# Optimization experiments

Measured on AMD Instinct MI355X. Metric: run time of the kernel, lower is better.

## Reference

```python
import jax, jax.numpy as jnp
import numpy as np

N, F, C, H, D = 32768, 128, 4, 8, 32
DM = H * D  # 256, d_model
E, B = 65536, 8192


def _pe():
    # sinusoidal positional encoding over the chain dimension, shape [C, DM]
    pos = jnp.arange(C, dtype=jnp.float32)[:, None]
    di = jnp.arange(0, DM, 2, dtype=jnp.float32)[None, :]
    div = 10000.0 ** (di / DM)
    pe = jnp.zeros((C, DM), jnp.float32)
    pe = pe.at[:, 0::2].set(jnp.sin(pos / div))
    pe = pe.at[:, 1::2].set(jnp.cos(pos / div))
    return pe


def _leaky(v):
    return jnp.where(v >= 0, v, 0.2 * v)


def setup_inputs() -> dict:
    key = jax.random.key(0)
    ks = jax.random.split(key, 6)
    x = jax.random.normal(ks[0], (N, F), jnp.float32)
    edge_index = jax.random.randint(ks[1], (2, E), 0, N)
    bridge_index = jax.random.randint(ks[2], (2, B), 0, N)
    W_in = jax.random.normal(ks[3], (DM, F), jnp.float32) * 0.05       # linear_input.weight
    double_attn = jax.random.normal(ks[4], (1, C * H, D), jnp.float32) * 0.1
    W_res = jax.random.normal(ks[5], (C * DM, F), jnp.float32) * 0.05  # residual_linear.weight
    bias = jnp.zeros((C * DM,), jnp.float32)
    prelu_w = jnp.float32(0.25)  # nn.PReLU default
    return {"x": x, "edge_index": edge_index, "bridge_index": bridge_index,
            "W_in": W_in, "double_attn": double_attn, "W_res": W_res,
            "bias": bias, "prelu_w": prelu_w}


def reference(x, edge_index, bridge_index, W_in, double_attn, W_res, bias, prelu_w):
    n = x.shape[0]
    # project + chain positional encoding -> [n, C, H, D]
    xl = x @ W_in.T                                   # [n, DM]
    xr = (xl[:, None, :] + _pe()[None]).reshape(n, C, H, D)

    src_bond, dst_bond = edge_index[0], edge_index[1]
    bond_attn = _leaky(xr[src_bond] + xr[dst_bond])   # [E, C, H, D]

    src_bridge, dst_bridge = bridge_index[0], bridge_index[1]
    ch = jnp.arange(C)
    prev_ch = jnp.clip(ch - 1, 0, None)
    next_ch = jnp.clip(ch + 1, None, C - 1)
    src2dst = _leaky(xr[dst_bridge] + xr[src_bridge][:, next_ch]).at[:, -1].set(0.0)
    dst2src = _leaky(xr[src_bridge] + xr[dst_bridge][:, prev_ch]).at[:, 0].set(0.0)

    full_src = jnp.concatenate([src_bond, src_bridge, dst_bridge])   # [Et]
    full_dst = jnp.concatenate([dst_bond, dst_bridge, src_bridge])   # [Et]
    x_src = jnp.concatenate([xr[src_bond], xr[src_bridge], xr[dst_bridge]], axis=0).reshape(-1, C * H, D)
    edge_attn = jnp.concatenate([bond_attn, src2dst, dst2src], axis=0).reshape(-1, C * H, D)

    scores = (double_attn * edge_attn).sum(-1)        # [Et, C*H]
    exp_s = jnp.exp(scores - scores.max())            # global-max stabilized, as in original
    denom = jax.ops.segment_sum(exp_s, full_dst, num_segments=n)     # [n, C*H]
    alpha = exp_s / (denom[full_dst] + 1e-16)

    # NOTE: faithful to original bug - x_src (per-edge, len Et) indexed by NODE ids
    proj = x_src[full_src] * alpha[..., None]         # [Et, C*H, D]
    out = jax.ops.segment_sum(proj, full_dst, num_segments=n)        # [n, C*H, D]

    out = out + (x @ W_res.T).reshape(n, C * H, D)    # residual
    out = out.reshape(n, C * H * D) + bias            # concat + bias
    out = jnp.where(out >= 0, out, prelu_w * out)     # PReLU
    return out
```

## Files before the change

kernel.cpp:

```cpp
#include <hip/hip_runtime.h>
#include <math.h>

#define N_NODES 32768
#define F_IN    128
#define C_CH    4
#define H_HEADS 8
#define D_DIM   32
#define DM      256
#define E_BOND  65536
#define B_BRIDGE 8192
#define ET      (E_BOND + 2*B_BRIDGE)
#define OUTC    1024
#define CAP     24
#define NCOLS   1280

#define WS_XL      0u
#define WS_PE      33554432u
#define WS_SCORES  33558528u
#define WS_BUCKET2 44044288u
#define WS_CNT     50335744u
#define WS_GMAX    50466816u
#define WS_RESID   50470912u
#define WS_XB      117579776u
#define WS_WC      125968384u

typedef __attribute__((ext_vector_type(8))) short bf16x8;
typedef __attribute__((ext_vector_type(4))) float f32x4;
typedef __attribute__((ext_vector_type(4))) _Float16 f16x4;

__device__ __forceinline__ unsigned enc_f32(float f) {
    unsigned u = __float_as_uint(f);
    return (u & 0x80000000u) ? ~u : (u | 0x80000000u);
}
__device__ __forceinline__ float dec_f32(unsigned u) {
    return (u & 0x80000000u) ? __uint_as_float(u & 0x7fffffffu) : __uint_as_float(~u);
}
__device__ __forceinline__ float leaky(float v) { return v >= 0.f ? v : 0.2f*v; }
__device__ __forceinline__ ushort f2bf(float f) {
    unsigned u = __float_as_uint(f);
    unsigned r = (u + 0x7fffu + ((u >> 16) & 1u)) >> 16;
    return (ushort)r;
}

__device__ __forceinline__ void edge_decode(int e, const int* __restrict__ ei,
                                            const int* __restrict__ bi,
                                            int& nA, int& nB, int& tp) {
    if (e < E_BOND)               { nA = ei[e]; nB = ei[E_BOND + e]; tp = 0; }
    else if (e < E_BOND+B_BRIDGE) { int i = e - E_BOND;
                                    nA = bi[B_BRIDGE + i]; nB = bi[i]; tp = 1; }
    else                          { int i = e - E_BOND - B_BRIDGE;
                                    nA = bi[i]; nB = bi[B_BRIDGE + i]; tp = 2; }
}

__global__ void pe_init_kernel(float* __restrict__ pe, unsigned* __restrict__ gmax) {
    int tid = threadIdx.x;
    int c = tid >> 8, p = tid & 255;
    float expo = (float)(p & ~1) * (1.0f/256.0f);
    float div  = powf(10000.0f, expo);
    float arg  = (float)c / div;
    pe[tid] = (p & 1) ? cosf(arg) : sinf(arg);
    if (tid == 0) *gmax = 0u;
}

__global__ __launch_bounds__(256) void cvt_x_kernel(const float* __restrict__ x,
                                                    ushort* __restrict__ xb) {
    const long i = (long)blockIdx.x*256 + threadIdx.x;
    float4 v = ((const float4*)x)[i];
    ushort4 o; o.x = f2bf(v.x); o.y = f2bf(v.y); o.z = f2bf(v.z); o.w = f2bf(v.w);
    ((ushort4*)xb)[i] = o;
}
__global__ __launch_bounds__(256) void cvt_w_kernel(const float* __restrict__ W_in,
                                                    const float* __restrict__ W_res,
                                                    ushort* __restrict__ wc) {
    const int i = blockIdx.x*256 + threadIdx.x;
    float4 v = (i < 8192) ? ((const float4*)W_in)[i] : ((const float4*)W_res)[i - 8192];
    ushort4 o; o.x = f2bf(v.x); o.y = f2bf(v.y); o.z = f2bf(v.z); o.w = f2bf(v.w);
    ((ushort4*)wc)[i] = o;
}

#define LDSK 72
__global__ __launch_bounds__(256) void mfma_gemm(
        const ushort* __restrict__ xb, const ushort* __restrict__ wc,
        float* __restrict__ xl, _Float16* __restrict__ resid) {
    __shared__ ushort As[128*LDSK];
    __shared__ ushort Bs[128*LDSK];
    const int tid = threadIdx.x;
    const int m0 = blockIdx.x * 128;
    const int n0 = blockIdx.y * 128;
    const int lane = tid & 63, wv = tid >> 6;
    const int wm = wv & 1, wn = wv >> 1;
    const int quad = lane >> 4, l15 = lane & 15;
    const int mbase = wm*64, nbase = wn*64;
    f32x4 acc[4][4] = {};

    for (int kt = 0; kt < 2; ++kt) {
        if (kt) __syncthreads();
#pragma unroll
        for (int i = 0; i < 4; ++i) {
            int c = tid + i*256;
            int row = c >> 3, seg = c & 7;
            *(uint4*)&As[row*LDSK + seg*8] =
                *(const uint4*)(xb + (long)(m0 + row)*F_IN + kt*64 + seg*8);
        }
#pragma unroll
        for (int i = 0; i < 4; ++i) {
            int c = tid + i*256;
            int row = c >> 3, seg = c & 7;
            *(uint4*)&Bs[row*LDSK + seg*8] =
                *(const uint4*)(wc + (long)(n0 + row)*F_IN + kt*64 + seg*8);
        }
        __syncthreads();
#pragma unroll
        for (int ks = 0; ks < 2; ++ks) {
            const int ko = ks*32 + quad*8;
            bf16x8 af[4], bfr[4];
#pragma unroll
            for (int mi = 0; mi < 4; ++mi)
                af[mi] = *(const bf16x8*)&As[(mbase + mi*16 + l15)*LDSK + ko];
#pragma unroll
            for (int ni = 0; ni < 4; ++ni)
                bfr[ni] = *(const bf16x8*)&Bs[(nbase + ni*16 + l15)*LDSK + ko];
#pragma unroll
            for (int mi = 0; mi < 4; ++mi)
#pragma unroll
                for (int ni = 0; ni < 4; ++ni)
                    acc[mi][ni] = __builtin_amdgcn_mfma_f32_16x16x32_bf16(
                        af[mi], bfr[ni], acc[mi][ni], 0, 0, 0);
        }
    }

    if (n0 < DM) {
#pragma unroll
        for (int mi = 0; mi < 4; ++mi) {
            const int mrow = m0 + mbase + mi*16 + quad*4;
#pragma unroll
            for (int ni = 0; ni < 4; ++ni) {
                const int col = n0 + nbase + ni*16 + l15;
#pragma unroll
                for (int r = 0; r < 4; ++r)
                    xl[(long)(mrow + r)*DM + col] = acc[mi][ni][r];
            }
        }
    } else {
        const int coloff = n0 - DM;
#pragma unroll
        for (int mi = 0; mi < 4; ++mi) {
            const int mrow = m0 + mbase + mi*16 + quad*4;
#pragma unroll
            for (int ni = 0; ni < 4; ++ni) {
                const int col = coloff + nbase + ni*16 + l15;
#pragma unroll
                for (int r = 0; r < 4; ++r)
                    resid[(long)(mrow + r)*OUTC + col] = (_Float16)acc[mi][ni][r];
            }
        }
    }
}

__global__ __launch_bounds__(256) void build_kernel(
        const int* __restrict__ ei, const int* __restrict__ bi,
        int* __restrict__ counts, int2* __restrict__ bucket2) {
    const int e = blockIdx.x*256 + threadIdx.x;
    if (e >= ET) return;
    int nA, nB, tp;
    edge_decode(e, ei, bi, nA, nB, tp);
    const int dst = (tp == 0) ? nB : nA;
    const int fs  = (tp == 0) ? nA : nB;
    const int g   = ei[fs];
    int slot = atomicAdd(&counts[dst], 1);
    if (slot < CAP) bucket2[dst*CAP + slot] = make_int2(e, g);
}

__global__ __launch_bounds__(256) void scores_kernel(
        const float* __restrict__ xl, const float* __restrict__ pe,
        const int* __restrict__ ei, const int* __restrict__ bi,
        const float* __restrict__ datt, float* __restrict__ scores,
        unsigned* __restrict__ gmax) {
    const int tid = threadIdx.x;
    const int l = tid & 63, wv = tid >> 6;
    const int pos = l * 4;
    const int h = l >> 3, dq = l & 7;

    float4 pe4[4], w4[4];
#pragma unroll
    for (int c = 0; c < 4; ++c) {
        pe4[c] = *(const float4*)(pe + c*DM + pos);
        w4[c]  = *(const float4*)(datt + (c*H_HEADS + h)*D_DIM + dq*4);
    }

    float wmax = -1e30f;
    const int wavebase = (blockIdx.x*4 + wv) * 8;
#pragma unroll
    for (int gdx = 0; gdx < 2; ++gdx) {
        const int e0 = wavebase + gdx*4;
        int nA[4], nB[4], tp[4];
#pragma unroll
        for (int j = 0; j < 4; ++j)
            edge_decode(e0 + j, ei, bi, nA[j], nB[j], tp[j]);
        float4 ua[4], ub[4];
#pragma unroll
        for (int j = 0; j < 4; ++j) {
            ua[j] = *(const float4*)(xl + (long)nA[j]*DM + pos);
            ub[j] = *(const float4*)(xl + (long)nB[j]*DM + pos);
        }
#pragma unroll
        for (int j = 0; j < 4; ++j) {
            const int e = e0 + j, t = tp[j];
            float sx = ua[j].x + ub[j].x;
            float sy = ua[j].y + ub[j].y;
            float sz = ua[j].z + ub[j].z;
            float sw = ua[j].w + ub[j].w;

            float p[4];
#pragma unroll
            for (int c = 0; c < 4; ++c) {
                int cB = (t == 0) ? c : (t == 1 ? (c+1 < 3 ? c+1 : 3)
                                               : (c-1 > 0 ? c-1 : 0));
                bool z = (t == 1 && c == 3) || (t == 2 && c == 0);
                float4 pa = pe4[c];
                float4 pb = (cB == 0) ? pe4[0] : (cB == 1) ? pe4[1]
                           : (cB == 2) ? pe4[2] : pe4[3];
                float v0 = leaky(sx + pa.x + pb.x);
                float v1 = leaky(sy + pa.y + pb.y);
                float v2 = leaky(sz + pa.z + pb.z);
                float v3 = leaky(sw + pa.w + pb.w);
                float d = w4[c].x*v0 + w4[c].y*v1 + w4[c].z*v2 + w4[c].w*v3;
                p[c] = z ? 0.f : d;
                p[c] += __shfl_xor(p[c], 1);
                p[c] += __shfl_xor(p[c], 2);
                p[c] += __shfl_xor(p[c], 4);
            }
            float val = (dq == 0) ? p[0] : (dq == 1) ? p[1] : (dq == 2) ? p[2] : p[3];
            if (dq < 4) scores[(long)e*32 + dq*8 + h] = val;
            wmax = fmaxf(wmax, fmaxf(fmaxf(p[0], p[1]), fmaxf(p[2], p[3])));
        }
    }

    wmax = fmaxf(wmax, __shfl_xor(wmax, 8));
    wmax = fmaxf(wmax, __shfl_xor(wmax, 16));
    wmax = fmaxf(wmax, __shfl_xor(wmax, 32));
    __shared__ float sm[4];
    if (l == 0) sm[wv] = wmax;
    __syncthreads();
    if (tid == 0) {
        float mm = fmaxf(fmaxf(sm[0], sm[1]), fmaxf(sm[2], sm[3]));
        atomicMax(gmax, enc_f32(mm));
    }
}

__global__ __launch_bounds__(256) void gather_kernel(
        const float* __restrict__ xl, const float* __restrict__ pe,
        const float* __restrict__ scores, const int* __restrict__ counts,
        const int2* __restrict__ bucket2, const _Float16* __restrict__ resid,
        const unsigned* __restrict__ gmax, const float* __restrict__ bias,
        const float* __restrict__ pw, float* __restrict__ out) {
    const int n = blockIdx.x;
    const int t = threadIdx.x;
    const int ch = t >> 3;
    const int d0 = (t & 7) * 4;
    const int h = ch & 7, c = ch >> 3;
    const int cnt = min(counts[n], CAP);
    const int col = ch*D_DIM + d0;
    const int nb = n*CAP;
    const float m = dec_f32(*gmax);

    const f16x4 hv = *(const f16x4*)(resid + (long)n*OUTC + col);
    const float4 b = *(const float4*)(bias + col);
    const float w = *pw;
    const float4 pv = *(const float4*)(pe + c*DM + h*D_DIM + d0);

    float4 acc = make_float4(0.f, 0.f, 0.f, 0.f);
    float esum = 0.f;

    for (int i0 = 0; i0 < cnt; i0 += 4) {
        int2 eg[4]; bool vld[4];
#pragma unroll
        for (int j = 0; j < 4; ++j) {
            const int idx = i0 + j;
            const int safe = idx < cnt ? idx : i0;
            eg[j] = bucket2[nb + safe];
            vld[j] = idx < cnt;
        }
        float sc[4];
#pragma unroll
        for (int j = 0; j < 4; ++j)
            sc[j] = scores[(long)eg[j].x*32 + ch];
        float4 xv[4];
#pragma unroll
        for (int j = 0; j < 4; ++j)
            xv[j] = *(const float4*)(xl + (long)eg[j].y*DM + h*D_DIM + d0);
#pragma unroll
        for (int j = 0; j < 4; ++j) {
            float ex = vld[j] ? __expf(sc[j] - m) : 0.f;
            acc.x += ex*xv[j].x; acc.y += ex*xv[j].y;
            acc.z += ex*xv[j].z; acc.w += ex*xv[j].w;
            esum += ex;
        }
    }
    const float inv = 1.f / (esum + 1e-16f);

    float r0 = (acc.x + esum*pv.x)*inv + (float)hv.x + b.x;
    float r1 = (acc.y + esum*pv.y)*inv + (float)hv.y + b.y;
    float r2 = (acc.z + esum*pv.z)*inv + (float)hv.z + b.z;
    float r3 = (acc.w + esum*pv.w)*inv + (float)hv.w + b.w;
    r0 = r0 >= 0.f ? r0 : w*r0;
    r1 = r1 >= 0.f ? r1 : w*r1;
    r2 = r2 >= 0.f ? r2 : w*r2;
    r3 = r3 >= 0.f ? r3 : w*r3;
    *(float4*)(out + (long)n*OUTC + col) = make_float4(r0, r1, r2, r3);
}

extern "C" void kernel_launch(void* const* d_in, const int* in_sizes, int n_in,
                              void* d_out, int out_size, void* d_ws, size_t ws_size,
                              hipStream_t stream) {
    const float* x     = (const float*)d_in[0];
    const int*   ei    = (const int*)d_in[1];
    const int*   bi    = (const int*)d_in[2];
    const float* W_in  = (const float*)d_in[3];
    const float* datt  = (const float*)d_in[4];
    const float* W_res = (const float*)d_in[5];
    const float* bias  = (const float*)d_in[6];
    const float* pw    = (const float*)d_in[7];
    float* out = (float*)d_out;
    char*  ws  = (char*)d_ws;

    float*     xl      = (float*)(ws + WS_XL);
    float*     pe      = (float*)(ws + WS_PE);
    float*     scores  = (float*)(ws + WS_SCORES);
    int2*      bucket2 = (int2*)(ws + WS_BUCKET2);
    int*       counts  = (int*)(ws + WS_CNT);
    unsigned*  gmax    = (unsigned*)(ws + WS_GMAX);
    _Float16*  resid   = (_Float16*)(ws + WS_RESID);
    ushort*    xb      = (ushort*)(ws + WS_XB);
    ushort*    wc      = (ushort*)(ws + WS_WC);

    hipMemsetAsync(counts, 0, (size_t)N_NODES*4, stream);
    pe_init_kernel<<<1, 1024, 0, stream>>>(pe, gmax);
    cvt_x_kernel<<<(N_NODES*F_IN/4)/256, 256, 0, stream>>>(x, xb);
    cvt_w_kernel<<<(NCOLS*F_IN/4 + 255)/256, 256, 0, stream>>>(W_in, W_res, wc);
    build_kernel<<<(ET+255)/256, 256, 0, stream>>>(ei, bi, counts, bucket2);
    {
        dim3 grid(N_NODES/128, NCOLS/128);
        mfma_gemm<<<grid, 256, 0, stream>>>(xb, wc, xl, resid);
    }
    scores_kernel<<<2560, 256, 0, stream>>>(xl, pe, ei, bi, datt, scores, gmax);
    gather_kernel<<<N_NODES, 256, 0, stream>>>(xl, pe, scores, counts, bucket2,
                                               resid, gmax, bias, pw, out);
}
```

Baseline: 321.7 us.

## Merge prep kernels and co-schedule residual GEMM with edge scoring

Four small setup kernels (pe init, x/W bf16 conversion, bucket build) become one multi-role launch. The GEMM is split so the xl projection runs first, and the residual GEMM tiles share a launch with the scores kernel. Blocks are interleaved 4 GEMM to 5 score blocks, so compute-bound MFMA work overlaps the memory-bound edge gathers. This cuts launch overhead and per-kernel tails, but the mixed kernel now reserves GEMM-sized LDS for every block, which may limit occupancy for the score blocks.

```diff
diff --git a/kernel.cpp b/kernel.cpp
--- a/kernel.cpp
+++ b/kernel.cpp
@@ -52,41 +52,60 @@
                                     nA = bi[i]; nB = bi[B_BRIDGE + i]; tp = 2; }
 }
 
-__global__ void pe_init_kernel(float* __restrict__ pe, unsigned* __restrict__ gmax) {
-    int tid = threadIdx.x;
-    int c = tid >> 8, p = tid & 255;
-    float expo = (float)(p & ~1) * (1.0f/256.0f);
-    float div  = powf(10000.0f, expo);
-    float arg  = (float)c / div;
-    pe[tid] = (p & 1) ? cosf(arg) : sinf(arg);
-    if (tid == 0) *gmax = 0u;
-}
-
-__global__ __launch_bounds__(256) void cvt_x_kernel(const float* __restrict__ x,
-                                                    ushort* __restrict__ xb) {
-    const long i = (long)blockIdx.x*256 + threadIdx.x;
-    float4 v = ((const float4*)x)[i];
-    ushort4 o; o.x = f2bf(v.x); o.y = f2bf(v.y); o.z = f2bf(v.z); o.w = f2bf(v.w);
-    ((ushort4*)xb)[i] = o;
-}
-__global__ __launch_bounds__(256) void cvt_w_kernel(const float* __restrict__ W_in,
-                                                    const float* __restrict__ W_res,
-                                                    ushort* __restrict__ wc) {
-    const int i = blockIdx.x*256 + threadIdx.x;
-    float4 v = (i < 8192) ? ((const float4*)W_in)[i] : ((const float4*)W_res)[i - 8192];
-    ushort4 o; o.x = f2bf(v.x); o.y = f2bf(v.y); o.z = f2bf(v.z); o.w = f2bf(v.w);
-    ((ushort4*)wc)[i] = o;
+__global__ __launch_bounds__(256) void prep_kernel(
+        const float* __restrict__ x, const float* __restrict__ W_in,
+        const float* __restrict__ W_res, const int* __restrict__ ei,
+        const int* __restrict__ bi, ushort* __restrict__ xb,
+        ushort* __restrict__ wc, int* __restrict__ counts,
+        int2* __restrict__ bucket2, float* __restrict__ pe,
+        unsigned* __restrict__ gmax) {
+    const int bid = blockIdx.x;
+    const int tid = threadIdx.x;
+    if (bid < 4096) {
+        const long i = (long)bid*256 + tid;
+        float4 v = ((const float4*)x)[i];
+        ushort4 o; o.x = f2bf(v.x); o.y = f2bf(v.y); o.z = f2bf(v.z); o.w = f2bf(v.w);
+        ((ushort4*)xb)[i] = o;
+    } else if (bid < 4256) {
+        const int i = (bid - 4096)*256 + tid;
+        float4 v = (i < 8192) ? ((const float4*)W_in)[i]
+                              : ((const float4*)W_res)[i - 8192];
+        ushort4 o; o.x = f2bf(v.x); o.y = f2bf(v.y); o.z = f2bf(v.z); o.w = f2bf(v.w);
+        ((ushort4*)wc)[i] = o;
+    } else if (bid < 4576) {
+        const int e = (bid - 4256)*256 + tid;
+        if (e < ET) {
+            int nA, nB, tp;
+            edge_decode(e, ei, bi, nA, nB, tp);
+            const int dst = (tp == 0) ? nB : nA;
+            const int fs  = (tp == 0) ? nA : nB;
+            const int g   = ei[fs];
+            int slot = atomicAdd(&counts[dst], 1);
+            if (slot < CAP) bucket2[dst*CAP + slot] = make_int2(e, g);
+        }
+    } else {
+#pragma unroll
+        for (int k = 0; k < 4; ++k) {
+            int idx = k*256 + tid;
+            int c = idx >> 8, p = idx & 255;
+            float expo = (float)(p & ~1) * (1.0f/256.0f);
+            float div  = powf(10000.0f, expo);
+            float arg  = (float)c / div;
+            pe[idx] = (p & 1) ? cosf(arg) : sinf(arg);
+        }
+        if (tid == 0) *gmax = 0u;
+    }
 }
 
 #define LDSK 72
-__global__ __launch_bounds__(256) void mfma_gemm(
+__global__ __launch_bounds__(256) void gemm_xl_kernel(
         const ushort* __restrict__ xb, const ushort* __restrict__ wc,
-        float* __restrict__ xl, _Float16* __restrict__ resid) {
+        float* __restrict__ xl) {
     __shared__ ushort As[128*LDSK];
     __shared__ ushort Bs[128*LDSK];
     const int tid = threadIdx.x;
-    const int m0 = blockIdx.x * 128;
-    const int n0 = blockIdx.y * 128;
+    const int m0 = (blockIdx.x & 255) * 128;
+    const int n0 = (blockIdx.x >> 8) * 128;
     const int lane = tid & 63, wv = tid >> 6;
     const int wm = wv & 1, wn = wv >> 1;
     const int quad = lane >> 4, l15 = lane & 15;
@@ -129,122 +148,158 @@
         }
     }
 
-    if (n0 < DM) {
-#pragma unroll
-        for (int mi = 0; mi < 4; ++mi) {
-            const int mrow = m0 + mbase + mi*16 + quad*4;
-#pragma unroll
-            for (int ni = 0; ni < 4; ++ni) {
-                const int col = n0 + nbase + ni*16 + l15;
-#pragma unroll
-                for (int r = 0; r < 4; ++r)
-                    xl[(long)(mrow + r)*DM + col] = acc[mi][ni][r];
-            }
-        }
-    } else {
-        const int coloff = n0 - DM;
-#pragma unroll
-        for (int mi = 0; mi < 4; ++mi) {
-            const int mrow = m0 + mbase + mi*16 + quad*4;
-#pragma unroll
-            for (int ni = 0; ni < 4; ++ni) {
-                const int col = coloff + nbase + ni*16 + l15;
-#pragma unroll
-                for (int r = 0; r < 4; ++r)
-                    resid[(long)(mrow + r)*OUTC + col] = (_Float16)acc[mi][ni][r];
-            }
+#pragma unroll
+    for (int mi = 0; mi < 4; ++mi) {
+        const int mrow = m0 + mbase + mi*16 + quad*4;
+#pragma unroll
+        for (int ni = 0; ni < 4; ++ni) {
+            const int col = n0 + nbase + ni*16 + l15;
+#pragma unroll
+            for (int r = 0; r < 4; ++r)
+                xl[(long)(mrow + r)*DM + col] = acc[mi][ni][r];
         }
     }
 }
 
-__global__ __launch_bounds__(256) void build_kernel(
-        const int* __restrict__ ei, const int* __restrict__ bi,
-        int* __restrict__ counts, int2* __restrict__ bucket2) {
-    const int e = blockIdx.x*256 + threadIdx.x;
-    if (e >= ET) return;
-    int nA, nB, tp;
-    edge_decode(e, ei, bi, nA, nB, tp);
-    const int dst = (tp == 0) ? nB : nA;
-    const int fs  = (tp == 0) ? nA : nB;
-    const int g   = ei[fs];
-    int slot = atomicAdd(&counts[dst], 1);
-    if (slot < CAP) bucket2[dst*CAP + slot] = make_int2(e, g);
-}
-
-__global__ __launch_bounds__(256) void scores_kernel(
+__global__ __launch_bounds__(256) void mix_kernel(
+        const ushort* __restrict__ xb, const ushort* __restrict__ wc,
+        _Float16* __restrict__ resid,
         const float* __restrict__ xl, const float* __restrict__ pe,
         const int* __restrict__ ei, const int* __restrict__ bi,
         const float* __restrict__ datt, float* __restrict__ scores,
         unsigned* __restrict__ gmax) {
+    __shared__ ushort As[128*LDSK];
+    __shared__ ushort Bs[128*LDSK];
+    __shared__ float sm4[4];
     const int tid = threadIdx.x;
-    const int l = tid & 63, wv = tid >> 6;
-    const int pos = l * 4;
-    const int h = l >> 3, dq = l & 7;
-
-    float4 pe4[4], w4[4];
-#pragma unroll
-    for (int c = 0; c < 4; ++c) {
-        pe4[c] = *(const float4*)(pe + c*DM + pos);
-        w4[c]  = *(const float4*)(datt + (c*H_HEADS + h)*D_DIM + dq*4);
-    }
-
-    float wmax = -1e30f;
-    const int wavebase = (blockIdx.x*4 + wv) * 8;
-#pragma unroll
-    for (int gdx = 0; gdx < 2; ++gdx) {
-        const int e0 = wavebase + gdx*4;
-        int nA[4], nB[4], tp[4];
-#pragma unroll
-        for (int j = 0; j < 4; ++j)
-            edge_decode(e0 + j, ei, bi, nA[j], nB[j], tp[j]);
-        float4 ua[4], ub[4];
-#pragma unroll
-        for (int j = 0; j < 4; ++j) {
-            ua[j] = *(const float4*)(xl + (long)nA[j]*DM + pos);
-            ub[j] = *(const float4*)(xl + (long)nB[j]*DM + pos);
-        }
-#pragma unroll
-        for (int j = 0; j < 4; ++j) {
-            const int e = e0 + j, t = tp[j];
-            float sx = ua[j].x + ub[j].x;
-            float sy = ua[j].y + ub[j].y;
-            float sz = ua[j].z + ub[j].z;
-            float sw = ua[j].w + ub[j].w;
-
-            float p[4];
-#pragma unroll
-            for (int c = 0; c < 4; ++c) {
-                int cB = (t == 0) ? c : (t == 1 ? (c+1 < 3 ? c+1 : 3)
-                                               : (c-1 > 0 ? c-1 : 0));
-                bool z = (t == 1 && c == 3) || (t == 2 && c == 0);
-                float4 pa = pe4[c];
-                float4 pb = (cB == 0) ? pe4[0] : (cB == 1) ? pe4[1]
-                           : (cB == 2) ? pe4[2] : pe4[3];
-                float v0 = leaky(sx + pa.x + pb.x);
-                float v1 = leaky(sy + pa.y + pb.y);
-                float v2 = leaky(sz + pa.z + pb.z);
-                float v3 = leaky(sw + pa.w + pb.w);
-                float d = w4[c].x*v0 + w4[c].y*v1 + w4[c].z*v2 + w4[c].w*v3;
-                p[c] = z ? 0.f : d;
-                p[c] += __shfl_xor(p[c], 1);
-                p[c] += __shfl_xor(p[c], 2);
-                p[c] += __shfl_xor(p[c], 4);
-            }
-            float val = (dq == 0) ? p[0] : (dq == 1) ? p[1] : (dq == 2) ? p[2] : p[3];
-            if (dq < 4) scores[(long)e*32 + dq*8 + h] = val;
-            wmax = fmaxf(wmax, fmaxf(fmaxf(p[0], p[1]), fmaxf(p[2], p[3])));
-        }
-    }
-
-    wmax = fmaxf(wmax, __shfl_xor(wmax, 8));
-    wmax = fmaxf(wmax, __shfl_xor(wmax, 16));
-    wmax = fmaxf(wmax, __shfl_xor(wmax, 32));
-    __shared__ float sm[4];
-    if (l == 0) sm[wv] = wmax;
-    __syncthreads();
-    if (tid == 0) {
-        float mm = fmaxf(fmaxf(sm[0], sm[1]), fmaxf(sm[2], sm[3]));
-        atomicMax(gmax, enc_f32(mm));
+    const int grp = blockIdx.x / 9, r9 = blockIdx.x % 9;
+    const int lane = tid & 63, wv = tid >> 6;
+
+    if (r9 >= 5) {
+        const int gb = grp*4 + (r9 - 5);
+        const int m0 = (gb >> 3) * 128;
+        const int coloff = (gb & 7) * 128;
+        const int wm = wv & 1, wn = wv >> 1;
+        const int quad = lane >> 4, l15 = lane & 15;
+        const int mbase = wm*64, nbase = wn*64;
+        f32x4 acc[4][4] = {};
+
+        for (int kt = 0; kt < 2; ++kt) {
+            if (kt) __syncthreads();
+#pragma unroll
+            for (int i = 0; i < 4; ++i) {
+                int c = tid + i*256;
+                int row = c >> 3, seg = c & 7;
+                *(uint4*)&As[row*LDSK + seg*8] =
+                    *(const uint4*)(xb + (long)(m0 + row)*F_IN + kt*64 + seg*8);
+            }
+#pragma unroll
+            for (int i = 0; i < 4; ++i) {
+                int c = tid + i*256;
+                int row = c >> 3, seg = c & 7;
+                *(uint4*)&Bs[row*LDSK + seg*8] =
+                    *(const uint4*)(wc + (long)(DM + coloff + row)*F_IN + kt*64 + seg*8);
+            }
+            __syncthreads();
+#pragma unroll
+            for (int ks = 0; ks < 2; ++ks) {
+                const int ko = ks*32 + quad*8;
+                bf16x8 af[4], bfr[4];
+#pragma unroll
+                for (int mi = 0; mi < 4; ++mi)
+                    af[mi] = *(const bf16x8*)&As[(mbase + mi*16 + l15)*LDSK + ko];
+#pragma unroll
+                for (int ni = 0; ni < 4; ++ni)
+                    bfr[ni] = *(const bf16x8*)&Bs[(nbase + ni*16 + l15)*LDSK + ko];
+#pragma unroll
+                for (int mi = 0; mi < 4; ++mi)
+#pragma unroll
+                    for (int ni = 0; ni < 4; ++ni)
+                        acc[mi][ni] = __builtin_amdgcn_mfma_f32_16x16x32_bf16(
+                            af[mi], bfr[ni], acc[mi][ni], 0, 0, 0);
+            }
+        }
+#pragma unroll
+        for (int mi = 0; mi < 4; ++mi) {
+            const int mrow = m0 + mbase + mi*16 + quad*4;
+#pragma unroll
+            for (int ni = 0; ni < 4; ++ni) {
+                const int col = coloff + nbase + ni*16 + l15;
+#pragma unroll
+                for (int rr = 0; rr < 4; ++rr)
+                    resid[(long)(mrow + rr)*OUTC + col] = (_Float16)acc[mi][ni][rr];
+            }
+        }
+    } else {
+        const int sb = grp*5 + r9;
+        const int pos = lane * 4;
+        const int h = lane >> 3, dq = lane & 7;
+
+        float4 pe4[4], w4[4];
+#pragma unroll
+        for (int c = 0; c < 4; ++c) {
+            pe4[c] = *(const float4*)(pe + c*DM + pos);
+            w4[c]  = *(const float4*)(datt + (c*H_HEADS + h)*D_DIM + dq*4);
+        }
+
+        float wmax = -1e30f;
+        const int wavebase = (sb*4 + wv) * 8;
+#pragma unroll
+        for (int gdx = 0; gdx < 2; ++gdx) {
+            const int e0 = wavebase + gdx*4;
+            int nA[4], nB[4], tp[4];
+#pragma unroll
+            for (int j = 0; j < 4; ++j)
+                edge_decode(e0 + j, ei, bi, nA[j], nB[j], tp[j]);
+            float4 ua[4], ub[4];
+#pragma unroll
+            for (int j = 0; j < 4; ++j) {
+                ua[j] = *(const float4*)(xl + (long)nA[j]*DM + pos);
+                ub[j] = *(const float4*)(xl + (long)nB[j]*DM + pos);
+            }
+#pragma unroll
+            for (int j = 0; j < 4; ++j) {
+                const int e = e0 + j, t = tp[j];
+                float sx = ua[j].x + ub[j].x;
+                float sy = ua[j].y + ub[j].y;
+                float sz = ua[j].z + ub[j].z;
+                float sw = ua[j].w + ub[j].w;
+
+                float p[4];
+#pragma unroll
+                for (int c = 0; c < 4; ++c) {
+                    int cB = (t == 0) ? c : (t == 1 ? (c+1 < 3 ? c+1 : 3)
+                                                   : (c-1 > 0 ? c-1 : 0));
+                    bool z = (t == 1 && c == 3) || (t == 2 && c == 0);
+                    float4 pa = pe4[c];
+                    float4 pb = (cB == 0) ? pe4[0] : (cB == 1) ? pe4[1]
+                               : (cB == 2) ? pe4[2] : pe4[3];
+                    float v0 = leaky(sx + pa.x + pb.x);
+                    float v1 = leaky(sy + pa.y + pb.y);
+                    float v2 = leaky(sz + pa.z + pb.z);
+                    float v3 = leaky(sw + pa.w + pb.w);
+                    float d = w4[c].x*v0 + w4[c].y*v1 + w4[c].z*v2 + w4[c].w*v3;
+                    p[c] = z ? 0.f : d;
+                    p[c] += __shfl_xor(p[c], 1);
+                    p[c] += __shfl_xor(p[c], 2);
+                    p[c] += __shfl_xor(p[c], 4);
+                }
+                float val = (dq == 0) ? p[0] : (dq == 1) ? p[1]
+                           : (dq == 2) ? p[2] : p[3];
+                if (dq < 4) scores[(long)e*32 + dq*8 + h] = val;
+                wmax = fmaxf(wmax, fmaxf(fmaxf(p[0], p[1]), fmaxf(p[2], p[3])));
+            }
+        }
+
+        wmax = fmaxf(wmax, __shfl_xor(wmax, 8));
+        wmax = fmaxf(wmax, __shfl_xor(wmax, 16));
+        wmax = fmaxf(wmax, __shfl_xor(wmax, 32));
+        if (lane == 0) sm4[wv] = wmax;
+        __syncthreads();
+        if (tid == 0) {
+            float mm = fmaxf(fmaxf(sm4[0], sm4[1]), fmaxf(sm4[2], sm4[3]));
+            atomicMax(gmax, enc_f32(mm));
+        }
     }
 }
 
@@ -335,15 +390,11 @@
     ushort*    wc      = (ushort*)(ws + WS_WC);
 
     hipMemsetAsync(counts, 0, (size_t)N_NODES*4, stream);
-    pe_init_kernel<<<1, 1024, 0, stream>>>(pe, gmax);
-    cvt_x_kernel<<<(N_NODES*F_IN/4)/256, 256, 0, stream>>>(x, xb);
-    cvt_w_kernel<<<(NCOLS*F_IN/4 + 255)/256, 256, 0, stream>>>(W_in, W_res, wc);
-    build_kernel<<<(ET+255)/256, 256, 0, stream>>>(ei, bi, counts, bucket2);
-    {
-        dim3 grid(N_NODES/128, NCOLS/128);
-        mfma_gemm<<<grid, 256, 0, stream>>>(xb, wc, xl, resid);
-    }
-    scores_kernel<<<2560, 256, 0, stream>>>(xl, pe, ei, bi, datt, scores, gmax);
+    prep_kernel<<<4577, 256, 0, stream>>>(x, W_in, W_res, ei, bi, xb, wc,
+                                          counts, bucket2, pe, gmax);
+    gemm_xl_kernel<<<512, 256, 0, stream>>>(xb, wc, xl);
+    mix_kernel<<<4608, 256, 0, stream>>>(xb, wc, resid, xl, pe, ei, bi, datt,
+                                         scores, gmax);
     gather_kernel<<<N_NODES, 256, 0, stream>>>(xl, pe, scores, counts, bucket2,
                                                resid, gmax, bias, pw, out);
 }
```

New measurement: 320.7 us. No clear change (-0.3%).
